# Performance work log

Hardware: AMD Instinct MI355X
Metric: run time of the kernel (lower is better)

## Reference

```python
import jax, jax.numpy as jnp
import numpy as np
from jax import lax

K = 8192
D = 256
BETA = 0.1
DECAY = 0.99
EPS = 1e-05


def setup_inputs() -> dict:
    key = jax.random.key(0)
    k1, k2, k3 = jax.random.split(key, 3)
    z_e = jax.random.normal(k1, (8, 2048, D), dtype=jnp.float32)
    codebook = jax.random.normal(k2, (K, D), dtype=jnp.float32)
    ema_cluster_size = jnp.zeros((K,), dtype=jnp.float32)
    ema_w = jax.random.normal(k3, (K, D), dtype=jnp.float32)
    return {"z_e": z_e, "codebook": codebook,
            "ema_cluster_size": ema_cluster_size, "ema_w": ema_w}


def reference(z_e, codebook, ema_cluster_size, ema_w):
    B, L, Dd = z_e.shape
    # squared-distance matrix (B, L, K): ||z||^2 - 2 z.C^T + ||c||^2
    dist = ((z_e ** 2).sum(-1, keepdims=True)
            - 2.0 * jnp.einsum('bld,kd->blk', z_e, codebook)
            + (codebook ** 2).sum(-1))
    codes = jnp.argmin(dist, axis=-1)          # (B, L) int
    z_q = codebook[codes]                      # gather (B, L, D)

    # training-mode EMA statistics (segment_sum == one_hot.T @ z_e, memory-light)
    flat_codes = codes.reshape(-1)
    flat_z = z_e.reshape(-1, Dd)
    n_i = jax.ops.segment_sum(jnp.ones(flat_codes.shape, dtype=z_e.dtype),
                              flat_codes, num_segments=K)
    dw = jax.ops.segment_sum(flat_z, flat_codes, num_segments=K)
    new_cluster_size = DECAY * ema_cluster_size + (1.0 - DECAY) * n_i
    new_ema_w = DECAY * ema_w + (1.0 - DECAY) * dw
    new_codebook = new_ema_w / (new_cluster_size + EPS)[:, None]

    # straight-through combine and commitment loss
    z_q_st = z_e + lax.stop_gradient(z_q - z_e)
    vq_loss = BETA * jnp.mean((z_e - lax.stop_gradient(z_q)) ** 2)
    return z_q_st, codes, vq_loss, new_codebook, new_cluster_size, new_ema_w
```

## Files before the change

### kernel.cpp

```cpp
#include <hip/hip_runtime.h>
#include <hip/hip_bf16.h>
#include <math.h>

#define N_ROWS 16384
#define DIM    256
#define KCODES 8192

#define OFF_ZQ    0
#define OFF_CODES 4194304
#define OFF_LOSS  4210688
#define OFF_CB    4210689
#define OFF_CS    6307841
#define OFF_EW    6316033
#define OUT_TOTAL 8413185

typedef __attribute__((ext_vector_type(8))) short bf16x8;
typedef __attribute__((ext_vector_type(4))) float f32x4;
typedef __attribute__((ext_vector_type(16))) float f32x16;

__device__ __forceinline__ void gll16(const void* g, void* l) {
  __builtin_amdgcn_global_load_lds(
      (const __attribute__((address_space(1))) unsigned int*)g,
      (__attribute__((address_space(3))) unsigned int*)l, 16, 0, 0);
}

__device__ __forceinline__ unsigned short f2bf(float x) {
  __hip_bfloat16 h = __float2bfloat16(x);
  return *reinterpret_cast<unsigned short*>(&h);
}

__device__ __forceinline__ unsigned umin32(unsigned a, unsigned b) { return a < b ? a : b; }
__device__ __forceinline__ unsigned umax32(unsigned a, unsigned b) { return a > b ? a : b; }

__global__ __launch_bounds__(256) void k_cvt(const float* __restrict__ src,
                                             unsigned short* __restrict__ dst,
                                             int n8) {
  int i = blockIdx.x * 256 + threadIdx.x;
  if (i >= n8) return;
  const float4 a = ((const float4*)src)[i * 2];
  const float4 b = ((const float4*)src)[i * 2 + 1];
  union { unsigned short u[8]; uint4 v; } o;
  o.u[0] = f2bf(a.x); o.u[1] = f2bf(a.y); o.u[2] = f2bf(a.z); o.u[3] = f2bf(a.w);
  o.u[4] = f2bf(b.x); o.u[5] = f2bf(b.y); o.u[6] = f2bf(b.z); o.u[7] = f2bf(b.w);
  ((uint4*)dst)[i] = o.v;
}

__global__ __launch_bounds__(256) void k_prep(const float* __restrict__ cb,
                                              unsigned short* __restrict__ cbt,
                                              float* __restrict__ cnormb) {
  const int tid = threadIdx.x;
  const int code = blockIdx.x * 8 + (tid >> 5);
  const int dq = tid & 31;
  const float4 v0 = *(const float4*)(cb + (size_t)code * 256 + dq * 8);
  const float4 v1 = *(const float4*)(cb + (size_t)code * 256 + dq * 8 + 4);
  union { unsigned short u[8]; uint4 q; } o;
  o.u[0] = f2bf(-2.f * v0.x); o.u[1] = f2bf(-2.f * v0.y);
  o.u[2] = f2bf(-2.f * v0.z); o.u[3] = f2bf(-2.f * v0.w);
  o.u[4] = f2bf(-2.f * v1.x); o.u[5] = f2bf(-2.f * v1.y);
  o.u[6] = f2bf(-2.f * v1.z); o.u[7] = f2bf(-2.f * v1.w);
  *(uint4*)(cbt + ((size_t)dq * 8192 + code) * 8) = o.q;
  float s = v0.x * v0.x + v0.y * v0.y + v0.z * v0.z + v0.w * v0.w +
            v1.x * v1.x + v1.y * v1.y + v1.z * v1.z + v1.w * v1.w;
#pragma unroll
  for (int off = 16; off >= 1; off >>= 1) s += __shfl_down(s, off);
  if ((tid & 31) == 0) cnormb[code] = s + 1024.0f;
}

__global__ __launch_bounds__(256, 2) void k_argmin(
    const unsigned short* __restrict__ zb,
    const unsigned short* __restrict__ cbt,
    const float* __restrict__ cnb,
    unsigned long long* __restrict__ partials) {
  __shared__ __align__(16) unsigned char lds[69632];

  const int tid = threadIdx.x;
  const int lane = tid & 63;
  const int w = tid >> 6;
  const int wc = w & 1;
  const int wr = w >> 1;
  const int hi = lane >> 5;
  const int l31 = lane & 31;
  const int chunk = blockIdx.x;
  const int r0 = blockIdx.y << 7;

  {
    const char* zgb = (const char*)zb + (size_t)r0 * 512;
#pragma unroll
    for (int it = 0; it < 16; ++it) {
      int s = it * 256 + tid;
      int row = s >> 5;
      int dql = (tid & 31) ^ (row & 31);
      gll16(zgb + row * 512 + dql * 16, lds + s * 16);
    }
    gll16((const char*)cnb + (size_t)chunk * 4096 + tid * 16,
          lds + 65536 + tid * 16);
  }
  asm volatile("s_waitcnt vmcnt(0)" ::: "memory");
  __builtin_amdgcn_s_barrier();
  __builtin_amdgcn_sched_barrier(0);

  bf16x8 zr0[16], zr1[16];
  {
    const int xr = l31 * 16;
    const int rb0 = (wr * 64 + l31) * 512;
    const int rb1 = (wr * 64 + 32 + l31) * 512;
    const int hx = hi * 16;
#pragma unroll
    for (int ks = 0; ks < 16; ++ks) {
      zr0[ks] = *(const bf16x8*)(lds + rb0 + ((ks * 32 + hx) ^ xr));
      zr1[ks] = *(const bf16x8*)(lds + rb1 + ((ks * 32 + hx) ^ xr));
    }
  }
  asm volatile("s_waitcnt lgkmcnt(0)" ::: "memory");
  __builtin_amdgcn_s_barrier();
  __builtin_amdgcn_sched_barrier(0);

  unsigned char* lcb = lds + tid * 16;
  const char* cgc = (const char*)cbt +
      ((size_t)(tid >> 7) * 131072 + (size_t)chunk * 16384 + (tid & 127) * 16);
  gll16(cgc + 0 * 262144, lcb + 0 * 4096);
  gll16(cgc + 1 * 262144, lcb + 1 * 4096);
  gll16(cgc + 2 * 262144, lcb + 2 * 4096);

  const unsigned char* afp = lds + hi * 2048 + (wc * 64 + l31) * 16;
  const unsigned wchi4 = (unsigned)(wc * 64 + hi * 4);

  unsigned k1_00 = 0xFFFFFFFFu, k2_00 = 0xFFFFFFFFu;
  unsigned k1_01 = 0xFFFFFFFFu, k2_01 = 0xFFFFFFFFu;
  unsigned k1_10 = 0xFFFFFFFFu, k2_10 = 0xFFFFFFFFu;
  unsigned k1_11 = 0xFFFFFFFFu, k2_11 = 0xFFFFFFFFu;
  f32x16 acc00, acc01, acc10, acc11;

#define KSTEP(ks, TAIL)                                                        \
  {                                                                            \
    if ((TAIL) && (ks) == 14) asm volatile("s_waitcnt vmcnt(1)" ::: "memory"); \
    else if ((TAIL) && (ks) == 15) asm volatile("s_waitcnt vmcnt(0)" ::: "memory"); \
    else asm volatile("s_waitcnt vmcnt(2)" ::: "memory");                      \
    __builtin_amdgcn_s_barrier();                                              \
    __builtin_amdgcn_sched_barrier(0);                                         \
    if ((ks) < 13) {                                                           \
      gll16(cgc + ((ks) + 3) * 262144, lcb + (((ks) + 3) & 3) * 4096);         \
    } else if (!(TAIL)) {                                                      \
      gll16(cgc + 2048 + ((ks) - 13) * 262144, lcb + (((ks) + 3) & 3) * 4096); \
    }                                                                          \
    bf16x8 a0 = *(const bf16x8*)(afp + ((ks) & 3) * 4096);                     \
    bf16x8 a1 = *(const bf16x8*)(afp + ((ks) & 3) * 4096 + 512);               \
    acc00 = __builtin_amdgcn_mfma_f32_32x32x16_bf16(a0, zr0[ks], acc00, 0, 0, 0); \
    acc01 = __builtin_amdgcn_mfma_f32_32x32x16_bf16(a0, zr1[ks], acc01, 0, 0, 0); \
    acc10 = __builtin_amdgcn_mfma_f32_32x32x16_bf16(a1, zr0[ks], acc10, 0, 0, 0); \
    acc11 = __builtin_amdgcn_mfma_f32_32x32x16_bf16(a1, zr1[ks], acc11, 0, 0, 0); \
  }

#define CTBODY(TAIL)                                                           \
  {                                                                            \
    const int cnoff = 65536 + ct * 512 + wc * 256 + hi * 16;                   \
    f32x4 cnA[4], cnB[4];                                                      \
    _Pragma("unroll") for (int g2 = 0; g2 < 4; ++g2) {                         \
      cnA[g2] = *(const f32x4*)(lds + cnoff + g2 * 32);                        \
      cnB[g2] = *(const f32x4*)(lds + cnoff + 128 + g2 * 32);                  \
    }                                                                          \
    _Pragma("unroll") for (int r = 0; r < 16; ++r) {                           \
      float vA = cnA[r >> 2][r & 3], vB = cnB[r >> 2][r & 3];                  \
      acc00[r] = vA; acc01[r] = vA; acc10[r] = vB; acc11[r] = vB;              \
    }                                                                          \
    KSTEP(0, TAIL)  KSTEP(1, TAIL)  KSTEP(2, TAIL)  KSTEP(3, TAIL)             \
    KSTEP(4, TAIL)  KSTEP(5, TAIL)  KSTEP(6, TAIL)  KSTEP(7, TAIL)             \
    KSTEP(8, TAIL)  KSTEP(9, TAIL)  KSTEP(10, TAIL) KSTEP(11, TAIL)            \
    KSTEP(12, TAIL) KSTEP(13, TAIL) KSTEP(14, TAIL) KSTEP(15, TAIL)            \
    const unsigned vb = (unsigned)(ct * 128) | wchi4;                          \
    _Pragma("unroll") for (int r = 0; r < 16; ++r) {                           \
      const unsigned ic = (unsigned)(8 * (r >> 2) + (r & 3));                  \
      unsigned key;                                                            \
      key = (__float_as_uint(acc00[r]) & 0xFFFFFC00u) | vb | ic;               \
      if (key < k1_00) { k2_00 = k1_00; k1_00 = key; } else if (key < k2_00) k2_00 = key; \
      key = (__float_as_uint(acc01[r]) & 0xFFFFFC00u) | vb | ic;               \
      if (key < k1_01) { k2_01 = k1_01; k1_01 = key; } else if (key < k2_01) k2_01 = key; \
      key = (__float_as_uint(acc10[r]) & 0xFFFFFC00u) | vb | ic | 32u;         \
      if (key < k1_10) { k2_10 = k1_10; k1_10 = key; } else if (key < k2_10) k2_10 = key; \
      key = (__float_as_uint(acc11[r]) & 0xFFFFFC00u) | vb | ic | 32u;         \
      if (key < k1_11) { k2_11 = k1_11; k1_11 = key; } else if (key < k2_11) k2_11 = key; \
    }                                                                          \
    cgc += 2048;                                                               \
  }

  for (int ct = 0; ct < 7; ++ct) CTBODY(false)
  { int ct = 7; CTBODY(true) }
#undef CTBODY
#undef KSTEP

#define FIN(K1V, K2V, ZF, CF)                                                  \
  {                                                                            \
    unsigned o1 = (unsigned)__shfl_xor((int)(K1V), 32);                        \
    unsigned o2 = (unsigned)__shfl_xor((int)(K2V), 32);                        \
    unsigned n1 = umin32((K1V), o1);                                           \
    unsigned n2 = umin32(umax32((K1V), o1), umin32((K2V), o2));                \
    if (lane < 32) {                                                           \
      int row = r0 + wr * 64 + (ZF) * 32 + l31;                                \
      partials[(size_t)row * 32 + (chunk * 4 + wc * 2 + (CF))] =               \
          ((unsigned long long)n2 << 32) | n1;                                 \
    }                                                                          \
  }
  FIN(k1_00, k2_00, 0, 0) FIN(k1_10, k2_10, 0, 1)
  FIN(k1_01, k2_01, 1, 0) FIN(k1_11, k2_11, 1, 1)
#undef FIN
}

__global__ __launch_bounds__(256) void k_reduce(
    const unsigned long long* __restrict__ partials, const float* __restrict__ z,
    const float* __restrict__ cb, float* __restrict__ out_codes,
    int* __restrict__ cnt) {
  const int row = blockIdx.x * 4 + (threadIdx.x >> 6);
  const int lane = threadIdx.x & 63;
  const int e = lane & 31;

  unsigned myK1 = 0xFFFFFFFFu, myK2 = 0xFFFFFFFFu;
  if (lane < 32) {
    unsigned long long v = partials[(size_t)row * 32 + e];
    myK1 = (unsigned)v; myK2 = (unsigned)(v >> 32);
  }
  unsigned K1 = myK1, K2 = myK2;
  int bc = e >> 2;
#pragma unroll
  for (int m = 1; m <= 32; m <<= 1) {
    unsigned o1 = (unsigned)__shfl_xor((int)K1, m);
    unsigned o2 = (unsigned)__shfl_xor((int)K2, m);
    int ob = __shfl_xor(bc, m);
    unsigned nK2 = umin32(umax32(K1, o1), umin32(K2, o2));
    if (o1 < K1 || (o1 == K1 && ob < bc)) { K1 = o1; bc = ob; }
    K2 = nK2;
  }
  int chosen = bc * 1024 + (int)(K1 & 1023u);

  float r1 = __uint_as_float(K1 & 0xFFFFFC00u);
  float r2 = __uint_as_float(K2 & 0xFFFFFC00u);
  if (r2 - r1 < 0.75f) {
    const float win = r1 + 0.75f;
    const float* zr = z + ((size_t)row << 8);
    double bestd = 1e300; int bestj = 0x7fffffff;
#pragma unroll
    for (int h = 0; h < 2; ++h) {
      unsigned k = h ? myK2 : myK1;
      float bv = __uint_as_float(k & 0xFFFFFC00u);
      if (lane < 32 && bv <= win) {
        int jv = (e >> 2) * 1024 + (int)(k & 1023u);
        const float* c = cb + ((size_t)jv << 8);
        double d = 0.0;
        for (int kk = 0; kk < DIM; ++kk) {
          double df = (double)zr[kk] - (double)c[kk];
          d += df * df;
        }
        if (d < bestd || (d == bestd && jv < bestj)) { bestd = d; bestj = jv; }
      }
    }
#pragma unroll
    for (int m = 1; m <= 32; m <<= 1) {
      double od = __shfl_xor(bestd, m);
      int oj = __shfl_xor(bestj, m);
      if (od < bestd || (od == bestd && oj < bestj)) { bestd = od; bestj = oj; }
    }
    chosen = bestj;
  }
  if (lane == 0) {
    out_codes[row] = (float)chosen;
    if (cnt) atomicAdd(&cnt[chosen], 1);
  }
}

__global__ __launch_bounds__(1024) void k_scan(
    const int* __restrict__ cnt, int* __restrict__ start,
    int* __restrict__ cursor, const float* __restrict__ ema_cs,
    float* __restrict__ cs_out) {
  __shared__ int ssum[1024];
  const int t = threadIdx.x;
  const int base = t * 8;
  int c[8], s = 0;
#pragma unroll
  for (int i = 0; i < 8; ++i) { c[i] = cnt[base + i]; s += c[i]; }
  ssum[t] = s;
  __syncthreads();
  for (int off = 1; off < 1024; off <<= 1) {
    int v = 0;
    if (t >= off) v = ssum[t - off];
    __syncthreads();
    ssum[t] += v;
    __syncthreads();
  }
  int ex = ssum[t] - s;
#pragma unroll
  for (int i = 0; i < 8; ++i) {
    start[base + i] = ex;
    cursor[base + i] = ex;
    cs_out[base + i] = 0.99f * ema_cs[base + i] + 0.01f * (float)c[i];
    ex += c[i];
  }
}

__global__ __launch_bounds__(256) void k_place(const float* __restrict__ codesf,
                                               int* __restrict__ cursor,
                                               int* __restrict__ rowlist) {
  int i = blockIdx.x * 256 + threadIdx.x;
  int c = (int)codesf[i];
  int p = atomicAdd(&cursor[c], 1);
  rowlist[p] = i;
}

__global__ __launch_bounds__(256) void k_dw2(
    const float* __restrict__ z, const float* __restrict__ cb,
    const int* __restrict__ start, const int* __restrict__ cnt,
    const int* __restrict__ rowlist, const float* __restrict__ ema_w,
    const float* __restrict__ cs_new, float* __restrict__ zq,
    float* __restrict__ ew, float* __restrict__ cb_out,
    float* __restrict__ loss_part) {
  const int k = blockIdx.x;
  const int d = threadIdx.x;
  const int s = start[k], n = cnt[k];
  const size_t o = ((size_t)k << 8) + d;
  const float q = cb[o];
  float a0 = 0.f, a1 = 0.f, a2 = 0.f, a3 = 0.f;
  float l0 = 0.f, l1 = 0.f, l2 = 0.f, l3 = 0.f;
  int t = 0;
  for (; t + 4 <= n; t += 4) {
    size_t ro0 = ((size_t)rowlist[s + t] << 8) + d;
    size_t ro1 = ((size_t)rowlist[s + t + 1] << 8) + d;
    size_t ro2 = ((size_t)rowlist[s + t + 2] << 8) + d;
    size_t ro3 = ((size_t)rowlist[s + t + 3] << 8) + d;
    float z0 = z[ro0], z1 = z[ro1], z2 = z[ro2], z3 = z[ro3];
    zq[ro0] = q; zq[ro1] = q; zq[ro2] = q; zq[ro3] = q;
    a0 += z0; a1 += z1; a2 += z2; a3 += z3;
    float d0 = z0 - q, d1 = z1 - q, d2 = z2 - q, d3 = z3 - q;
    l0 += d0 * d0; l1 += d1 * d1; l2 += d2 * d2; l3 += d3 * d3;
  }
  for (; t < n; ++t) {
    size_t ro = ((size_t)rowlist[s + t] << 8) + d;
    float zv = z[ro];
    zq[ro] = q;
    a0 += zv;
    float df = zv - q;
    l0 += df * df;
  }
  float a = (a0 + a1) + (a2 + a3);
  float lacc = (l0 + l1) + (l2 + l3);
  const float v = 0.99f * ema_w[o] + 0.01f * a;
  ew[o] = v;
  cb_out[o] = v / (cs_new[k] + 1e-5f);

#pragma unroll
  for (int off = 32; off >= 1; off >>= 1) lacc += __shfl_down(lacc, off);
  __shared__ float wp[4];
  if ((d & 63) == 0) wp[d >> 6] = lacc;
  __syncthreads();
  if (d == 0 && n > 0) {
    float ssum = (wp[0] + wp[1]) + (wp[2] + wp[3]);
    atomicAdd(loss_part + (k & 255), ssum * (float)(0.1 / 4194304.0));
  }
}

__global__ __launch_bounds__(256) void k_loss_final(
    const float* __restrict__ part, float* __restrict__ loss) {
  float s = part[threadIdx.x];
#pragma unroll
  for (int off = 32; off >= 1; off >>= 1) s += __shfl_down(s, off);
  __shared__ float w[4];
  if ((threadIdx.x & 63) == 0) w[threadIdx.x >> 6] = s;
  __syncthreads();
  if (threadIdx.x == 0) loss[0] = (w[0] + w[1]) + (w[2] + w[3]);
}

__global__ __launch_bounds__(256) void k_scatter(
    const float* __restrict__ z, const float* __restrict__ cb,
    const float* __restrict__ codesf, float* __restrict__ zq,
    float* __restrict__ loss, float* __restrict__ cs_acc,
    float* __restrict__ ew_acc) {
  const int row = blockIdx.x;
  const int d = threadIdx.x;
  const int c = (int)codesf[row];
  const float zv = z[((size_t)row << 8) + d];
  const float qv = cb[((size_t)c << 8) + d];
  zq[((size_t)row << 8) + d] = zv + (qv - zv);
  float diff = zv - qv;
  float sq = diff * diff;
#pragma unroll
  for (int off = 32; off >= 1; off >>= 1) sq += __shfl_down(sq, off);
  __shared__ float wpart[4];
  if ((d & 63) == 0) wpart[d >> 6] = sq;
  __syncthreads();
  if (d == 0) {
    float s = (wpart[0] + wpart[1]) + (wpart[2] + wpart[3]);
    atomicAdd(loss, s * (float)(0.1 / 4194304.0));
    atomicAdd(cs_acc + c, 1.0f);
  }
  atomicAdd(ew_acc + ((size_t)c << 8) + d, zv);
}

__global__ __launch_bounds__(256) void k_ema_cs(const float* __restrict__ ema_cs,
                                                float* __restrict__ cs_io) {
  const int k = blockIdx.x * 256 + threadIdx.x;
  const float cnt = cs_io[k];
  cs_io[k] = 0.99f * ema_cs[k] + 0.01f * cnt;
}

__global__ __launch_bounds__(256) void k_ema_w(const float* __restrict__ ema_w,
                                               const float* __restrict__ cs_new,
                                               float* __restrict__ ew_io,
                                               float* __restrict__ cb_out) {
  const int i = blockIdx.x * 256 + threadIdx.x;
  const float dw = ew_io[i];
  const float v = 0.99f * ema_w[i] + 0.01f * dw;
  ew_io[i] = v;
  cb_out[i] = v / (cs_new[i >> 8] + 1e-5f);
}

extern "C" void kernel_launch(void* const* d_in, const int* in_sizes, int n_in,
                              void* d_out, int out_size, void* d_ws, size_t ws_size,
                              hipStream_t stream) {
  const float* z      = (const float*)d_in[0];
  const float* cb     = (const float*)d_in[1];
  const float* ema_cs = (const float*)d_in[2];
  const float* ema_w  = (const float*)d_in[3];
  float* out = (float*)d_out;

  float* o_zq    = out + OFF_ZQ;
  float* o_codes = out + OFF_CODES;
  float* o_loss  = out + OFF_LOSS;
  float* o_cb    = out + OFF_CB;
  float* o_cs    = out + OFF_CS;
  float* o_ew    = out + OFF_EW;

  uintptr_t zb_a  = ((uintptr_t)o_cb + 15) & ~(uintptr_t)15;
  uintptr_t cbt_a = ((uintptr_t)o_ew + 15) & ~(uintptr_t)15;
  unsigned short* zbuf = (unsigned short*)zb_a;
  unsigned short* cbt  = (unsigned short*)cbt_a;
  float* cnormb = (float*)(cbt_a + 4194304);
  unsigned long long* partials = (unsigned long long*)o_zq;

  const size_t ws_need = 4 * (8192 * 3 + 16384 + 256);
  const bool sorted = (ws_size >= ws_need);
  int* cnt      = (int*)d_ws;
  int* start    = cnt + 8192;
  int* cursor   = start + 8192;
  int* rowlist  = cursor + 8192;
  float* loss_part = (float*)(rowlist + 16384);

  if (sorted) (void)hipMemsetAsync(d_ws, 0, ws_need, stream);

  k_cvt <<<2048, 256, 0, stream>>>(z, zbuf, 524288);
  k_prep<<<1024, 256, 0, stream>>>(cb, cbt, cnormb);

  dim3 g(8, 128);
  k_argmin<<<g, 256, 0, stream>>>(zbuf, cbt, cnormb, partials);
  k_reduce<<<N_ROWS / 4, 256, 0, stream>>>(partials, z, cb, o_codes,
                                           sorted ? cnt : (int*)nullptr);

  if (sorted) {
    k_scan <<<1, 1024, 0, stream>>>(cnt, start, cursor, ema_cs, o_cs);
    k_place<<<64, 256, 0, stream>>>(o_codes, cursor, rowlist);
    k_dw2<<<KCODES, 256, 0, stream>>>(z, cb, start, cnt, rowlist, ema_w,
                                      o_cs, o_zq, o_ew, o_cb, loss_part);
    k_loss_final<<<1, 256, 0, stream>>>(loss_part, o_loss);
  } else {
    (void)hipMemsetAsync(o_loss, 0,
                         (size_t)(OUT_TOTAL - OFF_LOSS) * sizeof(float), stream);
    k_scatter<<<N_ROWS, 256, 0, stream>>>(z, cb, o_codes, o_zq, o_loss, o_cs,
                                          o_ew);
    k_ema_cs<<<KCODES / 256, 256, 0, stream>>>(ema_cs, o_cs);
    k_ema_w <<<KCODES * DIM / 256, 256, 0, stream>>>(ema_w, o_cs, o_ew, o_cb);
  }
}
```

Measured before the change: 161.5 us.

## Load codebook tiles straight to registers, shrink LDS, fuse memset, warp-shuffle scan

The argmin kernel stops staging codebook tiles through LDS with barriers and instead prefetches them directly into registers four k-steps ahead. Its z tile is now loaded in four 32-row phases, which cuts LDS from 68KB to 20KB and should allow more blocks per CU. MFMA issue is wrapped in s_setprio. The workspace memset is folded into extra k_cvt blocks, and the scan kernel uses wave shuffles instead of a barrier-heavy LDS scan. The tradeoff is more vector registers, uncoalesced per-wave global loads with no cross-wave reuse, and a serialised z-load prologue.

```diff
diff --git a/kernel.cpp b/kernel.cpp
--- a/kernel.cpp
+++ b/kernel.cpp
@@ -34,15 +34,21 @@
 
 __global__ __launch_bounds__(256) void k_cvt(const float* __restrict__ src,
                                              unsigned short* __restrict__ dst,
-                                             int n8) {
+                                             int n8, int* __restrict__ cnt,
+                                             float* __restrict__ loss_part) {
   int i = blockIdx.x * 256 + threadIdx.x;
-  if (i >= n8) return;
-  const float4 a = ((const float4*)src)[i * 2];
-  const float4 b = ((const float4*)src)[i * 2 + 1];
-  union { unsigned short u[8]; uint4 v; } o;
-  o.u[0] = f2bf(a.x); o.u[1] = f2bf(a.y); o.u[2] = f2bf(a.z); o.u[3] = f2bf(a.w);
-  o.u[4] = f2bf(b.x); o.u[5] = f2bf(b.y); o.u[6] = f2bf(b.z); o.u[7] = f2bf(b.w);
-  ((uint4*)dst)[i] = o.v;
+  if (i < n8) {
+    const float4 a = ((const float4*)src)[i * 2];
+    const float4 b = ((const float4*)src)[i * 2 + 1];
+    union { unsigned short u[8]; uint4 v; } o;
+    o.u[0] = f2bf(a.x); o.u[1] = f2bf(a.y); o.u[2] = f2bf(a.z); o.u[3] = f2bf(a.w);
+    o.u[4] = f2bf(b.x); o.u[5] = f2bf(b.y); o.u[6] = f2bf(b.z); o.u[7] = f2bf(b.w);
+    ((uint4*)dst)[i] = o.v;
+  } else if (cnt) {
+    int zi = i - n8;
+    if (zi < 8192) cnt[zi] = 0;
+    else if (zi < 8448) loss_part[zi - 8192] = 0.0f;
+  }
 }
 
 __global__ __launch_bounds__(256) void k_prep(const float* __restrict__ cb,
@@ -71,7 +77,7 @@
     const unsigned short* __restrict__ cbt,
     const float* __restrict__ cnb,
     unsigned long long* __restrict__ partials) {
-  __shared__ __align__(16) unsigned char lds[69632];
+  __shared__ __align__(16) unsigned char lds[20480];
 
   const int tid = threadIdx.x;
   const int lane = tid & 63;
@@ -83,48 +89,62 @@
   const int chunk = blockIdx.x;
   const int r0 = blockIdx.y << 7;
 
-  {
-    const char* zgb = (const char*)zb + (size_t)r0 * 512;
-#pragma unroll
-    for (int it = 0; it < 16; ++it) {
-      int s = it * 256 + tid;
-      int row = s >> 5;
-      int dql = (tid & 31) ^ (row & 31);
-      gll16(zgb + row * 512 + dql * 16, lds + s * 16);
+  gll16((const char*)cnb + (size_t)chunk * 4096 + tid * 16,
+        lds + 16384 + tid * 16);
+  const char* zgb = (const char*)zb + (size_t)r0 * 512;
+#pragma unroll
+  for (int it = 0; it < 4; ++it) {
+    int s = it * 256 + tid;
+    int row = s >> 5;
+    int dql = (s & 31) ^ row;
+    gll16(zgb + row * 512 + dql * 16, lds + s * 16);
+  }
+
+  bf16x8 zr0[16], zr1[16];
+#pragma unroll
+  for (int p = 0; p < 4; ++p) {
+    asm volatile("s_waitcnt vmcnt(0)" ::: "memory");
+    __builtin_amdgcn_s_barrier();
+    __builtin_amdgcn_sched_barrier(0);
+    if ((p >> 1) == wr) {
+      const int xr = l31 * 16;
+      const int rb = l31 * 512;
+      const int hx = hi * 16;
+      if ((p & 1) == 0) {
+#pragma unroll
+        for (int ks = 0; ks < 16; ++ks)
+          zr0[ks] = *(const bf16x8*)(lds + rb + ((ks * 32 + hx) ^ xr));
+      } else {
+#pragma unroll
+        for (int ks = 0; ks < 16; ++ks)
+          zr1[ks] = *(const bf16x8*)(lds + rb + ((ks * 32 + hx) ^ xr));
+      }
     }
-    gll16((const char*)cnb + (size_t)chunk * 4096 + tid * 16,
-          lds + 65536 + tid * 16);
-  }
-  asm volatile("s_waitcnt vmcnt(0)" ::: "memory");
-  __builtin_amdgcn_s_barrier();
-  __builtin_amdgcn_sched_barrier(0);
-
-  bf16x8 zr0[16], zr1[16];
-  {
-    const int xr = l31 * 16;
-    const int rb0 = (wr * 64 + l31) * 512;
-    const int rb1 = (wr * 64 + 32 + l31) * 512;
-    const int hx = hi * 16;
-#pragma unroll
-    for (int ks = 0; ks < 16; ++ks) {
-      zr0[ks] = *(const bf16x8*)(lds + rb0 + ((ks * 32 + hx) ^ xr));
-      zr1[ks] = *(const bf16x8*)(lds + rb1 + ((ks * 32 + hx) ^ xr));
+    asm volatile("s_waitcnt lgkmcnt(0)" ::: "memory");
+    __builtin_amdgcn_sched_barrier(0);
+    __builtin_amdgcn_s_barrier();
+    if (p < 3) {
+#pragma unroll
+      for (int it = 0; it < 4; ++it) {
+        int s = it * 256 + tid;
+        int row = s >> 5;
+        int dql = (s & 31) ^ row;
+        gll16(zgb + ((p + 1) * 32 + row) * 512 + dql * 16, lds + s * 16);
+      }
     }
   }
-  asm volatile("s_waitcnt lgkmcnt(0)" ::: "memory");
-  __builtin_amdgcn_s_barrier();
-  __builtin_amdgcn_sched_barrier(0);
-
-  unsigned char* lcb = lds + tid * 16;
-  const char* cgc = (const char*)cbt +
-      ((size_t)(tid >> 7) * 131072 + (size_t)chunk * 16384 + (tid & 127) * 16);
-  gll16(cgc + 0 * 262144, lcb + 0 * 4096);
-  gll16(cgc + 1 * 262144, lcb + 1 * 4096);
-  gll16(cgc + 2 * 262144, lcb + 2 * 4096);
-
-  const unsigned char* afp = lds + hi * 2048 + (wc * 64 + l31) * 16;
+
+  const char* cgc = (const char*)cbt + (size_t)hi * 131072 +
+                    ((size_t)chunk * 1024 + wc * 64 + l31) * 16;
+  bf16x8 p0[4], p1[4];
+#pragma unroll
+  for (int s = 0; s < 4; ++s) {
+    const char* ap = cgc + s * 262144;
+    p0[s] = *(const bf16x8*)ap;
+    p1[s] = *(const bf16x8*)(ap + 512);
+  }
+
   const unsigned wchi4 = (unsigned)(wc * 64 + hi * 4);
-
   unsigned k1_00 = 0xFFFFFFFFu, k2_00 = 0xFFFFFFFFu;
   unsigned k1_01 = 0xFFFFFFFFu, k2_01 = 0xFFFFFFFFu;
   unsigned k1_10 = 0xFFFFFFFFu, k2_10 = 0xFFFFFFFFu;
@@ -133,27 +153,24 @@
 
 #define KSTEP(ks, TAIL)                                                        \
   {                                                                            \
-    if ((TAIL) && (ks) == 14) asm volatile("s_waitcnt vmcnt(1)" ::: "memory"); \
-    else if ((TAIL) && (ks) == 15) asm volatile("s_waitcnt vmcnt(0)" ::: "memory"); \
-    else asm volatile("s_waitcnt vmcnt(2)" ::: "memory");                      \
-    __builtin_amdgcn_s_barrier();                                              \
-    __builtin_amdgcn_sched_barrier(0);                                         \
-    if ((ks) < 13) {                                                           \
-      gll16(cgc + ((ks) + 3) * 262144, lcb + (((ks) + 3) & 3) * 4096);         \
-    } else if (!(TAIL)) {                                                      \
-      gll16(cgc + 2048 + ((ks) - 13) * 262144, lcb + (((ks) + 3) & 3) * 4096); \
+    bf16x8 a0 = p0[(ks) & 3], a1 = p1[(ks) & 3];                               \
+    if (!(TAIL) || (ks) < 12) {                 \
+      const char* ap = cgc + (((ks) + 4) & 15) * 262144 +                      \
+                       ((((ks) + 4) >> 4) * 2048);                             \
+      p0[(ks) & 3] = *(const bf16x8*)ap;                                       \
+      p1[(ks) & 3] = *(const bf16x8*)(ap + 512);                               \
     }                                                                          \
-    bf16x8 a0 = *(const bf16x8*)(afp + ((ks) & 3) * 4096);                     \
-    bf16x8 a1 = *(const bf16x8*)(afp + ((ks) & 3) * 4096 + 512);               \
+    __builtin_amdgcn_s_setprio(1);                                             \
     acc00 = __builtin_amdgcn_mfma_f32_32x32x16_bf16(a0, zr0[ks], acc00, 0, 0, 0); \
     acc01 = __builtin_amdgcn_mfma_f32_32x32x16_bf16(a0, zr1[ks], acc01, 0, 0, 0); \
     acc10 = __builtin_amdgcn_mfma_f32_32x32x16_bf16(a1, zr0[ks], acc10, 0, 0, 0); \
     acc11 = __builtin_amdgcn_mfma_f32_32x32x16_bf16(a1, zr1[ks], acc11, 0, 0, 0); \
+    __builtin_amdgcn_s_setprio(0);                                             \
   }
 
 #define CTBODY(TAIL)                                                           \
   {                                                                            \
-    const int cnoff = 65536 + ct * 512 + wc * 256 + hi * 16;                   \
+    const int cnoff = 16384 + ct * 512 + wc * 256 + hi * 16;                   \
     f32x4 cnA[4], cnB[4];                                                      \
     _Pragma("unroll") for (int g2 = 0; g2 < 4; ++g2) {                         \
       cnA[g2] = *(const f32x4*)(lds + cnoff + g2 * 32);                        \
@@ -270,22 +287,33 @@
     const int* __restrict__ cnt, int* __restrict__ start,
     int* __restrict__ cursor, const float* __restrict__ ema_cs,
     float* __restrict__ cs_out) {
-  __shared__ int ssum[1024];
   const int t = threadIdx.x;
+  const int lane = t & 63, wid = t >> 6;
   const int base = t * 8;
   int c[8], s = 0;
 #pragma unroll
   for (int i = 0; i < 8; ++i) { c[i] = cnt[base + i]; s += c[i]; }
-  ssum[t] = s;
+  int inc = s;
+#pragma unroll
+  for (int off = 1; off < 64; off <<= 1) {
+    int v = __shfl_up(inc, off);
+    if (lane >= off) inc += v;
+  }
+  __shared__ int wsum[16], wbase[16];
+  if (lane == 63) wsum[wid] = inc;
   __syncthreads();
-  for (int off = 1; off < 1024; off <<= 1) {
-    int v = 0;
-    if (t >= off) v = ssum[t - off];
-    __syncthreads();
-    ssum[t] += v;
-    __syncthreads();
-  }
-  int ex = ssum[t] - s;
+  if (t < 16) {
+    int v = wsum[t];
+    int winc = v;
+#pragma unroll
+    for (int off = 1; off < 16; off <<= 1) {
+      int u = __shfl_up(winc, off);
+      if (t >= off) winc += u;
+    }
+    wbase[t] = winc - v;
+  }
+  __syncthreads();
+  int ex = wbase[wid] + (inc - s);
 #pragma unroll
   for (int i = 0; i < 8; ++i) {
     start[base + i] = ex;
@@ -441,9 +469,8 @@
   int* rowlist  = cursor + 8192;
   float* loss_part = (float*)(rowlist + 16384);
 
-  if (sorted) (void)hipMemsetAsync(d_ws, 0, ws_need, stream);
-
-  k_cvt <<<2048, 256, 0, stream>>>(z, zbuf, 524288);
+  k_cvt <<<2081, 256, 0, stream>>>(z, zbuf, 524288,
+                                   sorted ? cnt : (int*)nullptr, loss_part);
   k_prep<<<1024, 256, 0, stream>>>(cb, cbt, cnormb);
 
   dim3 g(8, 128);
```

New measurement: 162.3 us. Within noise of the previous version (+0.4%).
